# Optimization experiments

Hardware: AMD Instinct MI355X
Metric: run time of the kernel (lower is better)

The kernel has to match this reference:

```python
import jax, jax.numpy as jnp
import numpy as np

B, S, H, N_IN, N_PROC, R = 4, 1024, 1024, 64, 16, 128

def setup_inputs() -> dict:
    key = jax.random.key(0)
    k0, k1, k2, k3, k4 = jax.random.split(key, 5)
    intermediate = jax.random.normal(k0, (B, S, H), dtype=jnp.float32)
    enriched_activations = jax.random.normal(k1, (B, S, N_IN), dtype=jnp.float32)
    # Conv2d(1 -> N_proc, kernel=(5, N_in)), default PyTorch init scale ~ 1/sqrt(fan_in)
    fan_in = 1 * 5 * N_IN
    conv_w = jax.random.uniform(k2, (N_PROC, 1, 5, N_IN), dtype=jnp.float32,
                                minval=-1.0, maxval=1.0) / np.sqrt(fan_in).astype(np.float32)
    conv_b = jnp.zeros((N_PROC,), dtype=jnp.float32)
    down_proj = 0.02 * jax.random.normal(k3, (N_PROC, H, R), dtype=jnp.float32)
    up_proj = 0.02 * jax.random.normal(k4, (N_PROC, R, H), dtype=jnp.float32)
    return {"intermediate": intermediate, "enriched_activations": enriched_activations,
            "conv_w": conv_w, "conv_b": conv_b, "down_proj": down_proj, "up_proj": up_proj}

def reference(intermediate, enriched_activations, conv_w, conv_b, down_proj, up_proj):
    # act_map: [B, 1, S, N_in]; conv kernel (5, N_in) with padding (2, 0) -> [B, N_proc, S, 1]
    act_map = enriched_activations[:, None, :, :]
    pr = jax.lax.conv_general_dilated(
        act_map, conv_w, window_strides=(1, 1), padding=((2, 2), (0, 0)),
        dimension_numbers=("NCHW", "OIHW", "NCHW"))
    pr = pr + conv_b[None, :, None, None]
    # squeeze width, transpose to [B, S, N_proc], sigmoid gate
    process_activations = jax.nn.sigmoid(jnp.transpose(pr[..., 0], (0, 2, 1)))
    # per-expert low-rank transform
    down = jnp.einsum("bsh,nhr->bsnr", intermediate, down_proj)          # [B,S,N,R]
    transformed = jnp.einsum("bsnr,nrh->bsnh", down, up_proj)            # [B,S,N,H]
    # gate-weighted sum over experts (fuses multiply + sum over n)
    output = jnp.einsum("bsnh,bsn->bsh", transformed, process_activations)
    return (output, process_activations)
```

## Files before the change

kernel.cpp:

```cpp
#include <hip/hip_runtime.h>
#include <hip/hip_fp16.h>

#define T_TOK 4096
#define H_DIM 1024
#define NIN   64
#define NP    16
#define R_DIM 128
#define S_DIM 1024
#define N1    (NP * R_DIM)

typedef _Float16 half8  __attribute__((ext_vector_type(8)));
typedef _Float16 half4v __attribute__((ext_vector_type(4)));
typedef float    floatx4 __attribute__((ext_vector_type(4)));

typedef __attribute__((address_space(3))) unsigned char lds_u8_t;
typedef __attribute__((address_space(1))) unsigned char gbl_u8_t;

__device__ __forceinline__ void g2l16(const void* g, void* l) {
  __builtin_amdgcn_global_load_lds((const gbl_u8_t*)g, (lds_u8_t*)l, 16, 0, 0);
}

__global__ __launch_bounds__(256)
void gates_kernel(const float* __restrict__ enr, const float* __restrict__ cw,
                  const float* __restrict__ cb, float* __restrict__ gates) {
  __shared__ float sw[NP][321];
  __shared__ float se[20][NIN];
  const int tid = threadIdx.x;
  const int t0 = blockIdx.x * 16;
  const int b  = t0 / S_DIM;
  const int s0 = t0 % S_DIM;
  for (int i = tid; i < NP * 320; i += 256) sw[i / 320][i % 320] = cw[i];
  for (int i = tid; i < 20 * NIN; i += 256) {
    int r = i >> 6, c = i & 63;
    int s = s0 + r - 2;
    se[r][c] = (s >= 0 && s < S_DIM) ? enr[((size_t)b * S_DIM + s) * NIN + c] : 0.f;
  }
  __syncthreads();
  const int lt = tid >> 4, n = tid & 15;
  float acc = cb[n];
  #pragma unroll
  for (int dh = 0; dh < 5; ++dh) {
    const float* wrow = &sw[n][dh * 64];
    const float* erow = se[lt + dh];
    #pragma unroll
    for (int j = 0; j < NIN; ++j) acc += erow[j] * wrow[j];
  }
  gates[(size_t)(t0 + lt) * NP + n] = 1.f / (1.f + expf(-acc));
}

__global__ __launch_bounds__(256)
void cast_f2h(const float* __restrict__ src, _Float16* __restrict__ dst, int n4) {
  int i = blockIdx.x * 256 + threadIdx.x;
  if (i >= n4) return;
  float4 v = reinterpret_cast<const float4*>(src)[i];
  half4v o;
  o[0] = (_Float16)v.x; o[1] = (_Float16)v.y; o[2] = (_Float16)v.z; o[3] = (_Float16)v.w;
  reinterpret_cast<half4v*>(dst)[i] = o;
}

__global__ __launch_bounds__(256)
void transpose_cast(const float* __restrict__ src, _Float16* __restrict__ dst,
                    int rows, int cols, long sblk, long dblk) {
  src += (size_t)blockIdx.z * sblk;
  dst += (size_t)blockIdx.z * dblk;
  __shared__ float tile[32][33];
  const int c0 = blockIdx.x * 32, r0 = blockIdx.y * 32;
  const int tx = threadIdx.x & 31, ty = threadIdx.x >> 5;
  #pragma unroll
  for (int k = 0; k < 32; k += 8)
    tile[ty + k][tx] = src[(size_t)(r0 + ty + k) * cols + c0 + tx];
  __syncthreads();
  #pragma unroll
  for (int k = 0; k < 32; k += 8)
    dst[(size_t)(c0 + ty + k) * rows + r0 + tx] = (_Float16)tile[tx][ty + k];
}

template <int BM, int GATE>
__global__ __launch_bounds__(256)
void gemm_bt(const _Float16* __restrict__ A, const _Float16* __restrict__ BT,
             const float* __restrict__ gates, void* __restrict__ Cv,
             const int N, const int K) {
  constexpr int BN = 128;
  constexpr int WM = BM / 2;
  constexpr int WN = BN / 2;
  constexpr int MI = WM / 16;
  constexpr int NJ = WN / 16;
  constexpr int CA = BM / 64;
  constexpr int CB = BN / 64;
  __shared__ _Float16 sA[BM * 32];
  __shared__ _Float16 sB[BN * 32];

  const int tid  = threadIdx.x;
  const int wave = tid >> 6, lane = tid & 63;
  const int m0 = blockIdx.y * BM, n0 = blockIdx.x * BN;
  const int wr = (wave >> 1) * WM, wc = (wave & 1) * WN;
  const int sub = lane >> 2;
  const int kc  = (lane & 3) * 8;
  const int fr = lane & 15, quad = lane >> 4;

  const _Float16* gA = A  + (size_t)(m0 + (wave * CA) * 16 + sub) * K + kc;
  const _Float16* gB = BT + (size_t)(n0 + (wave * CB) * 16 + sub) * K + kc;
  _Float16* lA = sA + (wave * CA) * 512;
  _Float16* lB = sB + (wave * CB) * 512;

  floatx4 acc[MI][NJ];
  #pragma unroll
  for (int i = 0; i < MI; ++i)
    #pragma unroll
    for (int j = 0; j < NJ; ++j) acc[i][j] = (floatx4)0.f;

  for (int k0 = 0; k0 < K; k0 += 32) {
    __syncthreads();
    #pragma unroll
    for (int c = 0; c < CA; ++c) g2l16(gA + (size_t)c * 16 * K + k0, lA + c * 512);
    #pragma unroll
    for (int c = 0; c < CB; ++c) g2l16(gB + (size_t)c * 16 * K + k0, lB + c * 512);
    __syncthreads();
    half8 af[MI], bfr[NJ];
    #pragma unroll
    for (int i = 0; i < MI; ++i)
      af[i] = *reinterpret_cast<const half8*>(&sA[(wr + i * 16 + fr) * 32 + quad * 8]);
    #pragma unroll
    for (int j = 0; j < NJ; ++j)
      bfr[j] = *reinterpret_cast<const half8*>(&sB[(wc + j * 16 + fr) * 32 + quad * 8]);
    #pragma unroll
    for (int i = 0; i < MI; ++i)
      #pragma unroll
      for (int j = 0; j < NJ; ++j)
        acc[i][j] = __builtin_amdgcn_mfma_f32_16x16x32_f16(af[i], bfr[j], acc[i][j], 0, 0, 0);
  }

  if (GATE) {
    _Float16* C = (_Float16*)Cv;
    #pragma unroll
    for (int i = 0; i < MI; ++i) {
      #pragma unroll
      for (int r = 0; r < 4; ++r) {
        const int row = m0 + wr + i * 16 + quad * 4 + r;
        const float g = gates[row * NP + blockIdx.x];
        #pragma unroll
        for (int j = 0; j < NJ; ++j) {
          const int col = n0 + wc + j * 16 + fr;
          C[(size_t)row * N + col] = (_Float16)(acc[i][j][r] * g);
        }
      }
    }
  } else {
    float* C = (float*)Cv;
    #pragma unroll
    for (int i = 0; i < MI; ++i)
      #pragma unroll
      for (int r = 0; r < 4; ++r) {
        const int row = m0 + wr + i * 16 + quad * 4 + r;
        #pragma unroll
        for (int j = 0; j < NJ; ++j) {
          const int col = n0 + wc + j * 16 + fr;
          C[(size_t)row * N + col] = acc[i][j][r];
        }
      }
  }
}

extern "C" void kernel_launch(void* const* d_in, const int* in_sizes, int n_in,
                              void* d_out, int out_size, void* d_ws, size_t ws_size,
                              hipStream_t stream) {
  const float* inter = (const float*)d_in[0];
  const float* enr   = (const float*)d_in[1];
  const float* convw = (const float*)d_in[2];
  const float* convb = (const float*)d_in[3];
  const float* dproj = (const float*)d_in[4];
  const float* uproj = (const float*)d_in[5];
  float* out   = (float*)d_out;
  float* gates = out + (size_t)T_TOK * H_DIM;

  _Float16* Xh  = (_Float16*)d_ws;
  _Float16* BT1 = Xh  + (size_t)T_TOK * H_DIM;
  _Float16* UT  = BT1 + (size_t)N1 * H_DIM;
  _Float16* Dsc = UT  + (size_t)H_DIM * N1;

  gates_kernel<<<T_TOK / 16, 256, 0, stream>>>(enr, convw, convb, gates);
  cast_f2h<<<(T_TOK * H_DIM / 4) / 256, 256, 0, stream>>>(inter, Xh, T_TOK * H_DIM / 4);
  transpose_cast<<<dim3(R_DIM / 32, H_DIM / 32, NP), 256, 0, stream>>>(
      dproj, BT1, H_DIM, R_DIM, (long)H_DIM * R_DIM, (long)H_DIM * R_DIM);
  transpose_cast<<<dim3(H_DIM / 32, N1 / 32, 1), 256, 0, stream>>>(
      uproj, UT, N1, H_DIM, 0, 0);
  gemm_bt<128, 1><<<dim3(N1 / 128, T_TOK / 128), 256, 0, stream>>>(
      Xh, BT1, gates, (void*)Dsc, N1, H_DIM);
  gemm_bt<64, 0><<<dim3(H_DIM / 128, T_TOK / 64), 256, 0, stream>>>(
      Dsc, UT, nullptr, (void*)out, H_DIM, N1);
}
```

Before: 166.1 us.

## Merge prep kernels into one launch and use BK=64 XOR-swizzled GEMM tiles

Replaces the four prep launches (gate conv, fp32-to-fp16 cast, and two weight transposes) with a single block-indexed prep kernel, which removes launch gaps and lets the independent prep work run at the same time. In the GEMM, the K tile doubles from 32 to 64 and the LDS layout gets an XOR swizzle on 16-byte chunks, which halves the number of barrier pairs per K and is meant to avoid LDS bank conflicts on fragment reads. The cost is more LDS per block, which may lower occupancy, and a merged kernel that allocates the larger shared buffer for every block.

```diff
diff --git a/kernel.cpp b/kernel.cpp
--- a/kernel.cpp
+++ b/kernel.cpp
@@ -20,52 +20,69 @@
   __builtin_amdgcn_global_load_lds((const gbl_u8_t*)g, (lds_u8_t*)l, 16, 0, 0);
 }
 
-__global__ __launch_bounds__(256)
-void gates_kernel(const float* __restrict__ enr, const float* __restrict__ cw,
-                  const float* __restrict__ cb, float* __restrict__ gates) {
-  __shared__ float sw[NP][321];
-  __shared__ float se[20][NIN];
-  const int tid = threadIdx.x;
-  const int t0 = blockIdx.x * 16;
-  const int b  = t0 / S_DIM;
-  const int s0 = t0 % S_DIM;
-  for (int i = tid; i < NP * 320; i += 256) sw[i / 320][i % 320] = cw[i];
-  for (int i = tid; i < 20 * NIN; i += 256) {
-    int r = i >> 6, c = i & 63;
-    int s = s0 + r - 2;
-    se[r][c] = (s >= 0 && s < S_DIM) ? enr[((size_t)b * S_DIM + s) * NIN + c] : 0.f;
-  }
-  __syncthreads();
-  const int lt = tid >> 4, n = tid & 15;
-  float acc = cb[n];
-  #pragma unroll
-  for (int dh = 0; dh < 5; ++dh) {
-    const float* wrow = &sw[n][dh * 64];
-    const float* erow = se[lt + dh];
-    #pragma unroll
-    for (int j = 0; j < NIN; ++j) acc += erow[j] * wrow[j];
-  }
-  gates[(size_t)(t0 + lt) * NP + n] = 1.f / (1.f + expf(-acc));
-}
+#define GATES_NB 256
+#define CAST_NB  4096
+#define DT_NB    2048
+#define UT_NB    2048
+#define PREP_NB  (GATES_NB + CAST_NB + DT_NB + UT_NB)
 
 __global__ __launch_bounds__(256)
-void cast_f2h(const float* __restrict__ src, _Float16* __restrict__ dst, int n4) {
-  int i = blockIdx.x * 256 + threadIdx.x;
-  if (i >= n4) return;
-  float4 v = reinterpret_cast<const float4*>(src)[i];
-  half4v o;
-  o[0] = (_Float16)v.x; o[1] = (_Float16)v.y; o[2] = (_Float16)v.z; o[3] = (_Float16)v.w;
-  reinterpret_cast<half4v*>(dst)[i] = o;
-}
+void prep_kernel(const float* __restrict__ enr, const float* __restrict__ cw,
+                 const float* __restrict__ cb, const float* __restrict__ inter,
+                 const float* __restrict__ dproj, const float* __restrict__ uproj,
+                 float* __restrict__ gates, _Float16* __restrict__ Xh,
+                 _Float16* __restrict__ BT1, _Float16* __restrict__ UT) {
+  __shared__ __align__(16) char smem_raw[25664];
+  const int tid = threadIdx.x;
+  int bx = blockIdx.x;
 
-__global__ __launch_bounds__(256)
-void transpose_cast(const float* __restrict__ src, _Float16* __restrict__ dst,
-                    int rows, int cols, long sblk, long dblk) {
-  src += (size_t)blockIdx.z * sblk;
-  dst += (size_t)blockIdx.z * dblk;
-  __shared__ float tile[32][33];
-  const int c0 = blockIdx.x * 32, r0 = blockIdx.y * 32;
-  const int tx = threadIdx.x & 31, ty = threadIdx.x >> 5;
+  if (bx < GATES_NB) {
+    float (*sw)[321] = (float (*)[321])smem_raw;
+    float (*se)[NIN] = (float (*)[NIN])(smem_raw + 20544);
+    const int t0 = bx * 16;
+    const int b = t0 / S_DIM, s0 = t0 % S_DIM;
+    for (int i = tid; i < NP * 320; i += 256) sw[i / 320][i % 320] = cw[i];
+    for (int i = tid; i < 20 * NIN; i += 256) {
+      int r = i >> 6, c = i & 63, s = s0 + r - 2;
+      se[r][c] = (s >= 0 && s < S_DIM) ? enr[((size_t)b * S_DIM + s) * NIN + c] : 0.f;
+    }
+    __syncthreads();
+    const int lt = tid >> 4, n = tid & 15;
+    float acc = cb[n];
+    #pragma unroll
+    for (int dh = 0; dh < 5; ++dh) {
+      const float* wrow = &sw[n][dh * 64];
+      const float* erow = se[lt + dh];
+      #pragma unroll
+      for (int j = 0; j < NIN; ++j) acc += erow[j] * wrow[j];
+    }
+    gates[(size_t)(t0 + lt) * NP + n] = 1.f / (1.f + expf(-acc));
+    return;
+  }
+  bx -= GATES_NB;
+  if (bx < CAST_NB) {
+    int i = bx * 256 + tid;
+    float4 v = reinterpret_cast<const float4*>(inter)[i];
+    half4v o;
+    o[0] = (_Float16)v.x; o[1] = (_Float16)v.y; o[2] = (_Float16)v.z; o[3] = (_Float16)v.w;
+    reinterpret_cast<half4v*>(Xh)[i] = o;
+    return;
+  }
+  bx -= CAST_NB;
+  const float* src; _Float16* dst; int rows, cols, bxt, byt;
+  if (bx < DT_NB) {
+    int n = bx >> 7, rem = bx & 127;
+    src = dproj + (size_t)n * H_DIM * R_DIM;
+    dst = BT1 + (size_t)n * R_DIM * H_DIM;
+    rows = H_DIM; cols = R_DIM; bxt = rem & 3; byt = rem >> 2;
+  } else {
+    bx -= DT_NB;
+    src = uproj; dst = UT; rows = N1; cols = H_DIM;
+    bxt = bx & 31; byt = bx >> 5;
+  }
+  float (*tile)[33] = (float (*)[33])smem_raw;
+  const int c0 = bxt * 32, r0 = byt * 32;
+  const int tx = tid & 31, ty = tid >> 5;
   #pragma unroll
   for (int k = 0; k < 32; k += 8)
     tile[ty + k][tx] = src[(size_t)(r0 + ty + k) * cols + c0 + tx];
@@ -80,28 +97,24 @@
 void gemm_bt(const _Float16* __restrict__ A, const _Float16* __restrict__ BT,
              const float* __restrict__ gates, void* __restrict__ Cv,
              const int N, const int K) {
-  constexpr int BN = 128;
-  constexpr int WM = BM / 2;
-  constexpr int WN = BN / 2;
-  constexpr int MI = WM / 16;
-  constexpr int NJ = WN / 16;
-  constexpr int CA = BM / 64;
-  constexpr int CB = BN / 64;
-  __shared__ _Float16 sA[BM * 32];
-  __shared__ _Float16 sB[BN * 32];
+  constexpr int BN = 128, BK = 64;
+  constexpr int WM = BM / 2, WN = BN / 2;
+  constexpr int MI = WM / 16, NJ = WN / 16;
+  constexpr int CA = BM / 32, CB = BN / 32;
+  __shared__ _Float16 sA[BM * BK];
+  __shared__ _Float16 sB[BN * BK];
 
-  const int tid  = threadIdx.x;
-  const int wave = tid >> 6, lane = tid & 63;
+  const int tid = threadIdx.x, wave = tid >> 6, lane = tid & 63;
   const int m0 = blockIdx.y * BM, n0 = blockIdx.x * BN;
   const int wr = (wave >> 1) * WM, wc = (wave & 1) * WN;
-  const int sub = lane >> 2;
-  const int kc  = (lane & 3) * 8;
+  const int rl = lane >> 3;
+  const int q  = (lane & 7) ^ rl;
   const int fr = lane & 15, quad = lane >> 4;
 
-  const _Float16* gA = A  + (size_t)(m0 + (wave * CA) * 16 + sub) * K + kc;
-  const _Float16* gB = BT + (size_t)(n0 + (wave * CB) * 16 + sub) * K + kc;
-  _Float16* lA = sA + (wave * CA) * 512;
-  _Float16* lB = sB + (wave * CB) * 512;
+  const _Float16* gA = A  + (size_t)(m0 + wave * CA * 8 + rl) * K + q * 8;
+  const _Float16* gB = BT + (size_t)(n0 + wave * CB * 8 + rl) * K + q * 8;
+  _Float16* lA = sA + wave * CA * 512;
+  _Float16* lB = sB + wave * CB * 512;
 
   floatx4 acc[MI][NJ];
   #pragma unroll
@@ -109,42 +122,43 @@
     #pragma unroll
     for (int j = 0; j < NJ; ++j) acc[i][j] = (floatx4)0.f;
 
-  for (int k0 = 0; k0 < K; k0 += 32) {
+  for (int k0 = 0; k0 < K; k0 += BK) {
     __syncthreads();
     #pragma unroll
-    for (int c = 0; c < CA; ++c) g2l16(gA + (size_t)c * 16 * K + k0, lA + c * 512);
+    for (int c = 0; c < CA; ++c) g2l16(gA + (size_t)c * 8 * K + k0, lA + c * 512);
     #pragma unroll
-    for (int c = 0; c < CB; ++c) g2l16(gB + (size_t)c * 16 * K + k0, lB + c * 512);
+    for (int c = 0; c < CB; ++c) g2l16(gB + (size_t)c * 8 * K + k0, lB + c * 512);
     __syncthreads();
-    half8 af[MI], bfr[NJ];
     #pragma unroll
-    for (int i = 0; i < MI; ++i)
-      af[i] = *reinterpret_cast<const half8*>(&sA[(wr + i * 16 + fr) * 32 + quad * 8]);
-    #pragma unroll
-    for (int j = 0; j < NJ; ++j)
-      bfr[j] = *reinterpret_cast<const half8*>(&sB[(wc + j * 16 + fr) * 32 + quad * 8]);
-    #pragma unroll
-    for (int i = 0; i < MI; ++i)
+    for (int h = 0; h < 2; ++h) {
+      const int sa = ((quad + 4 * h) ^ (fr & 7)) * 8;
+      half8 af[MI], bf[NJ];
+      #pragma unroll
+      for (int i = 0; i < MI; ++i)
+        af[i] = *reinterpret_cast<const half8*>(&sA[(wr + i * 16 + fr) * 64 + sa]);
       #pragma unroll
       for (int j = 0; j < NJ; ++j)
-        acc[i][j] = __builtin_amdgcn_mfma_f32_16x16x32_f16(af[i], bfr[j], acc[i][j], 0, 0, 0);
+        bf[j] = *reinterpret_cast<const half8*>(&sB[(wc + j * 16 + fr) * 64 + sa]);
+      #pragma unroll
+      for (int i = 0; i < MI; ++i)
+        #pragma unroll
+        for (int j = 0; j < NJ; ++j)
+          acc[i][j] = __builtin_amdgcn_mfma_f32_16x16x32_f16(af[i], bf[j], acc[i][j], 0, 0, 0);
+    }
   }
 
   if (GATE) {
     _Float16* C = (_Float16*)Cv;
     #pragma unroll
-    for (int i = 0; i < MI; ++i) {
+    for (int i = 0; i < MI; ++i)
       #pragma unroll
       for (int r = 0; r < 4; ++r) {
         const int row = m0 + wr + i * 16 + quad * 4 + r;
         const float g = gates[row * NP + blockIdx.x];
         #pragma unroll
-        for (int j = 0; j < NJ; ++j) {
-          const int col = n0 + wc + j * 16 + fr;
-          C[(size_t)row * N + col] = (_Float16)(acc[i][j][r] * g);
-        }
+        for (int j = 0; j < NJ; ++j)
+          C[(size_t)row * N + n0 + wc + j * 16 + fr] = (_Float16)(acc[i][j][r] * g);
       }
-    }
   } else {
     float* C = (float*)Cv;
     #pragma unroll
@@ -153,10 +167,8 @@
       for (int r = 0; r < 4; ++r) {
         const int row = m0 + wr + i * 16 + quad * 4 + r;
         #pragma unroll
-        for (int j = 0; j < NJ; ++j) {
-          const int col = n0 + wc + j * 16 + fr;
-          C[(size_t)row * N + col] = acc[i][j][r];
-        }
+        for (int j = 0; j < NJ; ++j)
+          C[(size_t)row * N + n0 + wc + j * 16 + fr] = acc[i][j][r];
       }
   }
 }
@@ -178,12 +190,8 @@
   _Float16* UT  = BT1 + (size_t)N1 * H_DIM;
   _Float16* Dsc = UT  + (size_t)H_DIM * N1;
 
-  gates_kernel<<<T_TOK / 16, 256, 0, stream>>>(enr, convw, convb, gates);
-  cast_f2h<<<(T_TOK * H_DIM / 4) / 256, 256, 0, stream>>>(inter, Xh, T_TOK * H_DIM / 4);
-  transpose_cast<<<dim3(R_DIM / 32, H_DIM / 32, NP), 256, 0, stream>>>(
-      dproj, BT1, H_DIM, R_DIM, (long)H_DIM * R_DIM, (long)H_DIM * R_DIM);
-  transpose_cast<<<dim3(H_DIM / 32, N1 / 32, 1), 256, 0, stream>>>(
-      uproj, UT, N1, H_DIM, 0, 0);
+  prep_kernel<<<PREP_NB, 256, 0, stream>>>(enr, convw, convb, inter, dproj, uproj,
+                                           gates, Xh, BT1, UT);
   gemm_bt<128, 1><<<dim3(N1 / 128, T_TOK / 128), 256, 0, stream>>>(
       Xh, BT1, gates, (void*)Dsc, N1, H_DIM);
   gemm_bt<64, 0><<<dim3(H_DIM / 128, T_TOK / 64), 256, 0, stream>>>(
```

Result: faster. 146.4 us (-11.9%).
